# Performance work log

Measured on AMD Instinct MI355X. Metric: run time of the kernel, lower is better.

The kernel has to match this reference:

```python
import jax, jax.numpy as jnp
import numpy as np

B, S, D = 4, 2048, 1024
E, H, K = 32, 128, 2


def setup_inputs() -> dict:
    key = jax.random.key(0)
    k1, k2, k3, k4 = jax.random.split(key, 4)
    scale_d = 1.0 / np.sqrt(D)
    scale_h = 1.0 / np.sqrt(H)
    return {
        "x": jax.random.normal(k1, (B, S, D), dtype=jnp.float32),
        "w_sel": jax.random.normal(k2, (E, D), dtype=jnp.float32) * scale_d,      # router Linear weight [E, D]
        "w_keys": jax.random.normal(k3, (E, D, H), dtype=jnp.float32) * scale_d,  # per-expert up-proj
        "w_values": jax.random.normal(k4, (E, H, D), dtype=jnp.float32) * scale_h, # per-expert down-proj
        "k": K,
    }


def reference(x, w_sel, w_keys, w_values, k):
    # Router: sigmoid gating + top-k expert selection per token.
    sel = jax.nn.sigmoid(jnp.einsum('bsd,ed->bse', x, w_sel))      # [B,S,E]
    sel_val, sel_idx = jax.lax.top_k(sel, k)                       # [B,S,k]
    n_exp = w_sel.shape[0]
    # Dense gate matrix: gate[b,s,e] = sum of sel_val over heads routed to e
    # (top_k indices are distinct, so this matches the per-head accumulation).
    gate = jnp.sum(jax.nn.one_hot(sel_idx, n_exp, dtype=x.dtype) * sel_val[..., None], axis=-2)  # [B,S,E]
    # Expert up-projection + ReLU for all experts (dense equivalent of the
    # per-token gathered keys[expert_idx](token); unselected experts are
    # zeroed by the gate so the math is identical).
    scores = jax.nn.relu(jnp.einsum('bsd,edh->bseh', x, w_keys))   # [B,S,E,H]
    weighted = scores * gate[..., None]                            # [B,S,E,H]
    out = jnp.einsum('bseh,ehd->bsd', weighted, w_values)          # [B,S,D]
    return out
```

## Files before the change

kernel.cpp:

```cpp
#include <hip/hip_runtime.h>
#include <cstdint>
#include <cstddef>

#define NTOK 8192
#define DIM  1024
#define NEXP 32
#define NH   128
#define TT   32
#define NSLOT 32
#define BK   128
#define RT   32
#define LCAP 1024
#define NRB  (NTOK / RT)

typedef __attribute__((ext_vector_type(8))) short short8;
typedef __attribute__((ext_vector_type(4))) float float4_;

static __device__ __forceinline__ unsigned short f2bf(float f) {
  unsigned u = __float_as_uint(f);
  return (unsigned short)((u + 0x7fffu + ((u >> 16) & 1u)) >> 16);
}
static __device__ __forceinline__ float bf2f(unsigned short h) {
  return __uint_as_float(((unsigned)h) << 16);
}
static __device__ __forceinline__ void gload_lds16(const unsigned short* g,
                                                   unsigned short* l) {
  __builtin_amdgcn_global_load_lds(
      (const __attribute__((address_space(1))) unsigned int*)(const void*)g,
      (__attribute__((address_space(3))) unsigned int*)(void*)l, 16, 0, 0);
}

__global__ __launch_bounds__(256) void prep_router_kernel(
    const float* __restrict__ x, const float* __restrict__ w_sel,
    const float* __restrict__ w_keys, const float* __restrict__ w_values,
    unsigned short* __restrict__ xbf, unsigned short* __restrict__ wk_t,
    unsigned short* __restrict__ wv_t,
    int* __restrict__ counts, unsigned* __restrict__ list)
{
  __shared__ __align__(16) char smem[22656];
  const int bid = blockIdx.x;
  const int tid = threadIdx.x;

  if (bid >= NRB) {
    float (*tile)[65] = (float (*)[65])smem;
    const int lb = bid - NRB;
    const float* src; unsigned short* dst; int R, C, e, t, tpc;
    if (lb < 1024) { src = w_keys;   dst = wk_t; R = DIM; C = NH;  e = lb >> 5;          t = lb & 31; tpc = 2; }
    else           { src = w_values; dst = wv_t; R = NH;  C = DIM; e = (lb - 1024) >> 5; t = (lb - 1024) & 31; tpc = 16; }
    const int r0 = (t / tpc) * 64;
    const int c0 = (t % tpc) * 64;
    const float* s = src + (size_t)e * R * C;
    unsigned short* d = dst + (size_t)e * R * C;

    const int i  = tid >> 2;
    const int j0 = (tid & 3) * 16;
    #pragma unroll
    for (int k4 = 0; k4 < 4; ++k4) {
      float4 v = *(const float4*)(s + (size_t)(r0 + i) * C + c0 + j0 + k4 * 4);
      tile[i][j0 + k4 * 4 + 0] = v.x;
      tile[i][j0 + k4 * 4 + 1] = v.y;
      tile[i][j0 + k4 * 4 + 2] = v.z;
      tile[i][j0 + k4 * 4 + 3] = v.w;
    }
    __syncthreads();
    unsigned pk[8];
    #pragma unroll
    for (int k = 0; k < 8; ++k) {
      unsigned lo = f2bf(tile[j0 + 2 * k][i]);
      unsigned hi = f2bf(tile[j0 + 2 * k + 1][i]);
      pk[k] = lo | (hi << 16);
    }
    uint4 u0; u0.x = pk[0]; u0.y = pk[1]; u0.z = pk[2]; u0.w = pk[3];
    uint4 u1; u1.x = pk[4]; u1.y = pk[5]; u1.z = pk[6]; u1.w = pk[7];
    unsigned short* dp = d + (size_t)(c0 + i) * R + r0 + j0;
    *(uint4*)(dp)     = u0;
    *(uint4*)(dp + 8) = u1;
    return;
  }

  float (*xs_t)[36] = (float (*)[36])smem;
  float (*ws_t)[36] = (float (*)[36])(smem + 9216);
  float (*S)[33]    = (float (*)[33])(smem + 18432);
  float (*red)[64][16] = (float (*)[64][16])smem;

  const int tok0 = bid * RT;
  const int wv   = tid >> 6;
  const int lane = tid & 63;
  const int tr   = tid >> 3;
  const int i8   = tid & 7;
  const int d8   = i8 * 8;
  const int swzW = i8 << 2;
  const int tg4  = (lane & 7) * 4;
  const int eg4  = (lane >> 3) * 4;
  const int dlo  = wv * 16;

  float acc[16];
  #pragma unroll
  for (int k = 0; k < 16; ++k) acc[k] = 0.f;

  float4 a0, a1, b0, b1;
  {
    const float* xp = x + (size_t)(tok0 + tr) * DIM + d8;
    a0 = *(const float4*)(xp);
    a1 = *(const float4*)(xp + 4);
    const float* wp = w_sel + (size_t)tr * DIM + d8;
    b0 = *(const float4*)(wp);
    b1 = *(const float4*)(wp + 4);
  }

  for (int c = 0; c < 16; ++c) {
    const int dc = c * 64;

    {
      const int colx = tr ^ swzW;
      xs_t[d8 + 0][colx] = a0.x; xs_t[d8 + 1][colx] = a0.y;
      xs_t[d8 + 2][colx] = a0.z; xs_t[d8 + 3][colx] = a0.w;
      xs_t[d8 + 4][colx] = a1.x; xs_t[d8 + 5][colx] = a1.y;
      xs_t[d8 + 6][colx] = a1.z; xs_t[d8 + 7][colx] = a1.w;
      ws_t[d8 + 0][colx] = b0.x; ws_t[d8 + 1][colx] = b0.y;
      ws_t[d8 + 2][colx] = b0.z; ws_t[d8 + 3][colx] = b0.w;
      ws_t[d8 + 4][colx] = b1.x; ws_t[d8 + 5][colx] = b1.y;
      ws_t[d8 + 6][colx] = b1.z; ws_t[d8 + 7][colx] = b1.w;
      uint4 u;
      u.x = (unsigned)f2bf(a0.x) | ((unsigned)f2bf(a0.y) << 16);
      u.y = (unsigned)f2bf(a0.z) | ((unsigned)f2bf(a0.w) << 16);
      u.z = (unsigned)f2bf(a1.x) | ((unsigned)f2bf(a1.y) << 16);
      u.w = (unsigned)f2bf(a1.z) | ((unsigned)f2bf(a1.w) << 16);
      *(uint4*)(xbf + (size_t)(tok0 + tr) * DIM + dc + d8) = u;
    }
    __syncthreads();

    if (c < 15) {
      const float* xp = x + (size_t)(tok0 + tr) * DIM + dc + 64 + d8;
      a0 = *(const float4*)(xp);
      a1 = *(const float4*)(xp + 4);
      const float* wp = w_sel + (size_t)tr * DIM + dc + 64 + d8;
      b0 = *(const float4*)(wp);
      b1 = *(const float4*)(wp + 4);
    }

    #pragma unroll
    for (int dd = 0; dd < 16; ++dd) {
      const int d  = dlo + dd;
      const int sz = (d >> 3) << 2;
      float4 xv = *(const float4*)&xs_t[d][tg4 ^ sz];
      float4 w4 = *(const float4*)&ws_t[d][eg4 ^ sz];
      acc[0]  = fmaf(w4.x, xv.x, acc[0]);  acc[1]  = fmaf(w4.x, xv.y, acc[1]);
      acc[2]  = fmaf(w4.x, xv.z, acc[2]);  acc[3]  = fmaf(w4.x, xv.w, acc[3]);
      acc[4]  = fmaf(w4.y, xv.x, acc[4]);  acc[5]  = fmaf(w4.y, xv.y, acc[5]);
      acc[6]  = fmaf(w4.y, xv.z, acc[6]);  acc[7]  = fmaf(w4.y, xv.w, acc[7]);
      acc[8]  = fmaf(w4.z, xv.x, acc[8]);  acc[9]  = fmaf(w4.z, xv.y, acc[9]);
      acc[10] = fmaf(w4.z, xv.z, acc[10]); acc[11] = fmaf(w4.z, xv.w, acc[11]);
      acc[12] = fmaf(w4.w, xv.x, acc[12]); acc[13] = fmaf(w4.w, xv.y, acc[13]);
      acc[14] = fmaf(w4.w, xv.z, acc[14]); acc[15] = fmaf(w4.w, xv.w, acc[15]);
    }
    __syncthreads();
  }

  #pragma unroll
  for (int ei = 0; ei < 4; ++ei) {
    float4 v; v.x = acc[ei * 4 + 0]; v.y = acc[ei * 4 + 1];
    v.z = acc[ei * 4 + 2]; v.w = acc[ei * 4 + 3];
    *(float4*)&red[wv][lane][ei * 4] = v;
  }
  __syncthreads();

  {
    const int eg2 = tid >> 5, tg2 = (tid >> 2) & 7, ei2 = tid & 3;
    const int cls = eg2 * 8 + tg2;
    float4 s4; s4.x = 0.f; s4.y = 0.f; s4.z = 0.f; s4.w = 0.f;
    #pragma unroll
    for (int w = 0; w < 4; ++w) {
      float4 v = *(const float4*)&red[w][cls][ei2 * 4];
      s4.x += v.x; s4.y += v.y; s4.z += v.z; s4.w += v.w;
    }
    S[tg2 * 4 + 0][eg2 * 4 + ei2] = s4.x;
    S[tg2 * 4 + 1][eg2 * 4 + ei2] = s4.y;
    S[tg2 * 4 + 2][eg2 * 4 + ei2] = s4.z;
    S[tg2 * 4 + 3][eg2 * 4 + ei2] = s4.w;
  }
  __syncthreads();

  if (tid < RT) {
    const int t = tid;
    float m1 = -1e30f, m2 = -1e30f;
    int i1 = 0, i2 = 0;
    for (int ee = 0; ee < NEXP; ++ee) {
      float v = S[t][ee];
      if (v > m1)      { m2 = m1; i2 = i1; m1 = v; i1 = ee; }
      else if (v > m2) { m2 = v; i2 = ee; }
    }
    const int token = tok0 + t;
    float g1 = 1.f / (1.f + __expf(-m1));
    float g2 = 1.f / (1.f + __expf(-m2));
    unsigned e1 = ((unsigned)f2bf(g1) << 16) | ((unsigned)token << 1);
    unsigned e2 = ((unsigned)f2bf(g2) << 16) | ((unsigned)token << 1) | 1u;
    int p1 = atomicAdd(&counts[i1], 1);
    if (p1 < LCAP) list[i1 * LCAP + p1] = e1;
    int p2 = atomicAdd(&counts[i2], 1);
    if (p2 < LCAP) list[i2 * LCAP + p2] = e2;
  }
}

__global__ __launch_bounds__(256, 4) void ffn_kernel(
    const unsigned short* __restrict__ xbf,
    const unsigned short* __restrict__ wk_t,
    const unsigned short* __restrict__ wv_t,
    float* __restrict__ out,
    unsigned short* __restrict__ cont,
    const int* __restrict__ counts, const unsigned* __restrict__ list,
    int use_cont)
{
  const int bid = blockIdx.x;
  const int e   = bid & 31;
  const int cnt = min(counts[e], LCAP);
  const int t0  = (bid >> 5) * TT;
  if (t0 >= cnt) return;

  __shared__ __align__(16) unsigned short uni[8448];
  __shared__ unsigned short ss[TT][NH + 8];
  __shared__ int   toks[TT];
  __shared__ float gates[TT];
  unsigned short (*xsf)[4096] = (unsigned short (*)[4096])uni;
  unsigned short (*st)[264]   = (unsigned short (*)[264])uni;

  const int tid  = threadIdx.x;
  const int wave = tid >> 6;
  const int lane = tid & 63;
  const int quad = lane >> 4;
  const int l16  = lane & 15;

  const unsigned short* wkb = wk_t + (size_t)e * NH * DIM;
  const unsigned short* wvb = wv_t + (size_t)e * DIM * NH;
  const int n_tok = min(TT, cnt - t0);

  if (tid < TT) {
    int valid = tid < n_tok;
    unsigned en = valid ? list[e * LCAP + t0 + tid] : 0u;
    toks[tid]  = valid ? (int)(en & 0xffffu) : -1;
    gates[tid] = valid ? bf2f((unsigned short)(en >> 16)) : 0.f;
  }
  __syncthreads();

  const int smt  = wave >> 1;
  const int skk0 = (wave & 1) * 2;
  {
    int sl   = toks[smt * 16 + l16];
    int gtok = (sl < 0) ? 0 : (sl >> 1);
    const unsigned short* gsrc = xbf + (size_t)gtok * DIM + quad * 8;

    #pragma unroll
    for (int i2 = 0; i2 < 2; ++i2)
      gload_lds16(gsrc + (skk0 + i2) * 32, &xsf[0][(smt * 4 + skk0 + i2) * 512]);
    __syncthreads();

    float4_ acc[2][2];
    #pragma unroll
    for (int mt = 0; mt < 2; ++mt)
      #pragma unroll
      for (int nt = 0; nt < 2; ++nt) acc[mt][nt] = (float4_){0.f, 0.f, 0.f, 0.f};

    for (int ci = 0; ci < 8; ++ci) {
      const int dc = ci * BK;
      if (ci < 7) {
        const int nb = (ci + 1) & 1;
        #pragma unroll
        for (int i2 = 0; i2 < 2; ++i2)
          gload_lds16(gsrc + dc + BK + (skk0 + i2) * 32,
                      &xsf[nb][(smt * 4 + skk0 + i2) * 512]);
      }
      short8 b[4][2];
      #pragma unroll
      for (int kk = 0; kk < 4; ++kk)
        #pragma unroll
        for (int nt = 0; nt < 2; ++nt)
          b[kk][nt] = *(const short8*)(wkb +
              (size_t)(wave * 32 + nt * 16 + l16) * DIM + dc + kk * 32 + quad * 8);

      const unsigned short* xb = &xsf[ci & 1][0];
      #pragma unroll
      for (int kk = 0; kk < 4; ++kk) {
        #pragma unroll
        for (int mt = 0; mt < 2; ++mt) {
          short8 a = *(const short8*)(xb + (mt * 4 + kk) * 512 + lane * 8);
          #pragma unroll
          for (int nt = 0; nt < 2; ++nt)
            acc[mt][nt] = __builtin_amdgcn_mfma_f32_16x16x32_bf16(a, b[kk][nt], acc[mt][nt], 0, 0, 0);
        }
      }
      __syncthreads();
    }

    #pragma unroll
    for (int mt = 0; mt < 2; ++mt)
      #pragma unroll
      for (int nt = 0; nt < 2; ++nt)
        #pragma unroll
        for (int r = 0; r < 4; ++r) {
          int row = mt * 16 + quad * 4 + r;
          float v = fmaxf(acc[mt][nt][r], 0.f) * gates[row];
          ss[row][wave * 32 + nt * 16 + l16] = f2bf(v);
        }
  }
  __syncthreads();

  #pragma unroll 1
  for (int nc = 0; nc < 4; ++nc) {
    const int colbase = wave * 256 + nc * 64;
    float4_ o[2][4];
    #pragma unroll
    for (int mt = 0; mt < 2; ++mt)
      #pragma unroll
      for (int nt = 0; nt < 4; ++nt) o[mt][nt] = (float4_){0.f, 0.f, 0.f, 0.f};

    #pragma unroll
    for (int kk = 0; kk < 4; ++kk) {
      short8 bk[4];
      #pragma unroll
      for (int nt = 0; nt < 4; ++nt)
        bk[nt] = *(const short8*)(wvb +
            (size_t)(colbase + nt * 16 + l16) * NH + kk * 32 + quad * 8);
      short8 a0 = *(const short8*)&ss[l16][kk * 32 + quad * 8];
      short8 a1 = *(const short8*)&ss[16 + l16][kk * 32 + quad * 8];
      #pragma unroll
      for (int nt = 0; nt < 4; ++nt) {
        o[0][nt] = __builtin_amdgcn_mfma_f32_16x16x32_bf16(a0, bk[nt], o[0][nt], 0, 0, 0);
        o[1][nt] = __builtin_amdgcn_mfma_f32_16x16x32_bf16(a1, bk[nt], o[1][nt], 0, 0, 0);
      }
    }

    if (use_cont) {
      #pragma unroll
      for (int mt = 0; mt < 2; ++mt)
        #pragma unroll
        for (int nt = 0; nt < 4; ++nt)
          #pragma unroll
          for (int r = 0; r < 4; ++r)
            st[mt * 16 + quad * 4 + r][wave * 64 + nt * 16 + l16] = f2bf(o[mt][nt][r]);
      __syncthreads();
      #pragma unroll
      for (int q = 0; q < 4; ++q) {
        int idx = q * 256 + tid;
        int row = idx >> 5, seg = idx & 31;
        if (row < n_tok) {
          int sl2 = toks[row];
          size_t base = ((size_t)((sl2 & 1) * NTOK + (sl2 >> 1))) * DIM
                        + (seg >> 3) * 256 + nc * 64 + (seg & 7) * 8;
          *(short8*)&cont[base] = *(const short8*)&st[row][seg * 8];
        }
      }
      __syncthreads();
    } else {
      #pragma unroll
      for (int mt = 0; mt < 2; ++mt)
        #pragma unroll
        for (int r = 0; r < 4; ++r) {
          int row = mt * 16 + quad * 4 + r;
          if (row < n_tok) {
            size_t base = (size_t)(toks[row] >> 1) * DIM + colbase;
            #pragma unroll
            for (int nt = 0; nt < 4; ++nt)
              unsafeAtomicAdd(&out[base + nt * 16 + l16], o[mt][nt][r]);
          }
        }
    }
  }
}

__global__ __launch_bounds__(256) void combine_kernel(
    const unsigned short* __restrict__ cont, float* __restrict__ out)
{
  size_t i = ((size_t)blockIdx.x * 256 + threadIdx.x) * 8;
  uint4 a = *(const uint4*)(cont + i);
  uint4 b = *(const uint4*)(cont + (size_t)NTOK * DIM + i);
  float4 r0, r1;
  r0.x = bf2f((unsigned short)(a.x & 0xffff)) + bf2f((unsigned short)(b.x & 0xffff));
  r0.y = bf2f((unsigned short)(a.x >> 16))    + bf2f((unsigned short)(b.x >> 16));
  r0.z = bf2f((unsigned short)(a.y & 0xffff)) + bf2f((unsigned short)(b.y & 0xffff));
  r0.w = bf2f((unsigned short)(a.y >> 16))    + bf2f((unsigned short)(b.y >> 16));
  r1.x = bf2f((unsigned short)(a.z & 0xffff)) + bf2f((unsigned short)(b.z & 0xffff));
  r1.y = bf2f((unsigned short)(a.z >> 16))    + bf2f((unsigned short)(b.z >> 16));
  r1.z = bf2f((unsigned short)(a.w & 0xffff)) + bf2f((unsigned short)(b.w & 0xffff));
  r1.w = bf2f((unsigned short)(a.w >> 16))    + bf2f((unsigned short)(b.w >> 16));
  *(float4*)(out + i) = r0;
  *(float4*)(out + i + 4) = r1;
}

extern "C" void kernel_launch(void* const* d_in, const int* in_sizes, int n_in,
                              void* d_out, int out_size, void* d_ws, size_t ws_size,
                              hipStream_t stream) {
  (void)in_sizes; (void)n_in;
  const float* x        = (const float*)d_in[0];
  const float* w_sel    = (const float*)d_in[1];
  const float* w_keys   = (const float*)d_in[2];
  const float* w_values = (const float*)d_in[3];
  float* out = (float*)d_out;

  char* ws = (char*)d_ws;
  size_t off = 0;
  int*            counts = (int*)(ws + off);            off += 4096;
  unsigned*       list   = (unsigned*)(ws + off);       off += (size_t)NEXP * LCAP * 4;
  unsigned short* wk_t   = (unsigned short*)(ws + off); off += (size_t)NEXP * NH * DIM * 2;
  unsigned short* wv_t   = (unsigned short*)(ws + off); off += (size_t)NEXP * NH * DIM * 2;
  unsigned short* xbf    = (unsigned short*)(ws + off); off += (size_t)NTOK * DIM * 2;
  unsigned short* cont   = (unsigned short*)(ws + off);
  size_t need_full = off + (size_t)2 * NTOK * DIM * 2;
  const int use_cont = (ws_size >= need_full) ? 1 : 0;

  hipMemsetAsync(counts, 0, NEXP * sizeof(int), stream);

  prep_router_kernel<<<NRB + 2048, 256, 0, stream>>>(x, w_sel, w_keys, w_values,
                                                     xbf, wk_t, wv_t, counts, list);

  if (!use_cont)
    hipMemsetAsync(out, 0, (size_t)out_size * sizeof(float), stream);

  ffn_kernel<<<NEXP * NSLOT, 256, 0, stream>>>(xbf, wk_t, wv_t, out, cont,
                                               counts, list, use_cont);

  if (use_cont)
    combine_kernel<<<NTOK * DIM / (256 * 8), 256, 0, stream>>>(cont, out);
}
```

Before: 212.2 us.

## Halve FFN token tile to 16 and move x bf16 conversion to separate blocks

```diff
diff --git a/kernel.cpp b/kernel.cpp
--- a/kernel.cpp
+++ b/kernel.cpp
@@ -6,12 +6,14 @@
 #define DIM  1024
 #define NEXP 32
 #define NH   128
-#define TT   32
-#define NSLOT 32
+#define TT   16
+#define NSLOT 64
 #define BK   128
 #define RT   32
 #define LCAP 1024
 #define NRB  (NTOK / RT)
+#define NTRB 2048
+#define NCVB 512
 
 typedef __attribute__((ext_vector_type(8))) short short8;
 typedef __attribute__((ext_vector_type(4))) float float4_;
@@ -41,6 +43,30 @@
   const int bid = blockIdx.x;
   const int tid = threadIdx.x;
 
+  if (bid >= NRB + NTRB) {
+    const int lb = bid - NRB - NTRB;
+    #pragma unroll
+    for (int q = 0; q < 4; ++q) {
+      const size_t off = (size_t)lb * 16384 + (size_t)q * 4096 + (size_t)tid * 16;
+      float4 v0 = *(const float4*)(x + off);
+      float4 v1 = *(const float4*)(x + off + 4);
+      float4 v2 = *(const float4*)(x + off + 8);
+      float4 v3 = *(const float4*)(x + off + 12);
+      uint4 u0, u1;
+      u0.x = (unsigned)f2bf(v0.x) | ((unsigned)f2bf(v0.y) << 16);
+      u0.y = (unsigned)f2bf(v0.z) | ((unsigned)f2bf(v0.w) << 16);
+      u0.z = (unsigned)f2bf(v1.x) | ((unsigned)f2bf(v1.y) << 16);
+      u0.w = (unsigned)f2bf(v1.z) | ((unsigned)f2bf(v1.w) << 16);
+      u1.x = (unsigned)f2bf(v2.x) | ((unsigned)f2bf(v2.y) << 16);
+      u1.y = (unsigned)f2bf(v2.z) | ((unsigned)f2bf(v2.w) << 16);
+      u1.z = (unsigned)f2bf(v3.x) | ((unsigned)f2bf(v3.y) << 16);
+      u1.w = (unsigned)f2bf(v3.z) | ((unsigned)f2bf(v3.w) << 16);
+      *(uint4*)(xbf + off)     = u0;
+      *(uint4*)(xbf + off + 8) = u1;
+    }
+    return;
+  }
+
   if (bid >= NRB) {
     float (*tile)[65] = (float (*)[65])smem;
     const int lb = bid - NRB;
@@ -121,12 +147,6 @@
       ws_t[d8 + 2][colx] = b0.z; ws_t[d8 + 3][colx] = b0.w;
       ws_t[d8 + 4][colx] = b1.x; ws_t[d8 + 5][colx] = b1.y;
       ws_t[d8 + 6][colx] = b1.z; ws_t[d8 + 7][colx] = b1.w;
-      uint4 u;
-      u.x = (unsigned)f2bf(a0.x) | ((unsigned)f2bf(a0.y) << 16);
-      u.y = (unsigned)f2bf(a0.z) | ((unsigned)f2bf(a0.w) << 16);
-      u.z = (unsigned)f2bf(a1.x) | ((unsigned)f2bf(a1.y) << 16);
-      u.w = (unsigned)f2bf(a1.z) | ((unsigned)f2bf(a1.w) << 16);
-      *(uint4*)(xbf + (size_t)(tok0 + tr) * DIM + dc + d8) = u;
     }
     __syncthreads();
 
@@ -217,11 +237,11 @@
   const int t0  = (bid >> 5) * TT;
   if (t0 >= cnt) return;
 
-  __shared__ __align__(16) unsigned short uni[8448];
+  __shared__ __align__(16) unsigned short uni[4224];
   __shared__ unsigned short ss[TT][NH + 8];
   __shared__ int   toks[TT];
   __shared__ float gates[TT];
-  unsigned short (*xsf)[4096] = (unsigned short (*)[4096])uni;
+  unsigned short (*xsf)[2048] = (unsigned short (*)[2048])uni;
   unsigned short (*st)[264]   = (unsigned short (*)[264])uni;
 
   const int tid  = threadIdx.x;
@@ -242,33 +262,23 @@
   }
   __syncthreads();
 
-  const int smt  = wave >> 1;
-  const int skk0 = (wave & 1) * 2;
   {
-    int sl   = toks[smt * 16 + l16];
+    int sl   = toks[l16];
     int gtok = (sl < 0) ? 0 : (sl >> 1);
     const unsigned short* gsrc = xbf + (size_t)gtok * DIM + quad * 8;
 
-    #pragma unroll
-    for (int i2 = 0; i2 < 2; ++i2)
-      gload_lds16(gsrc + (skk0 + i2) * 32, &xsf[0][(smt * 4 + skk0 + i2) * 512]);
+    gload_lds16(gsrc + wave * 32, &xsf[0][wave * 512]);
     __syncthreads();
 
-    float4_ acc[2][2];
-    #pragma unroll
-    for (int mt = 0; mt < 2; ++mt)
-      #pragma unroll
-      for (int nt = 0; nt < 2; ++nt) acc[mt][nt] = (float4_){0.f, 0.f, 0.f, 0.f};
+    float4_ acc[2];
+    acc[0] = (float4_){0.f, 0.f, 0.f, 0.f};
+    acc[1] = (float4_){0.f, 0.f, 0.f, 0.f};
 
     for (int ci = 0; ci < 8; ++ci) {
       const int dc = ci * BK;
-      if (ci < 7) {
-        const int nb = (ci + 1) & 1;
-        #pragma unroll
-        for (int i2 = 0; i2 < 2; ++i2)
-          gload_lds16(gsrc + dc + BK + (skk0 + i2) * 32,
-                      &xsf[nb][(smt * 4 + skk0 + i2) * 512]);
-      }
+      if (ci < 7)
+        gload_lds16(gsrc + dc + BK + wave * 32, &xsf[(ci + 1) & 1][wave * 512]);
+
       short8 b[4][2];
       #pragma unroll
       for (int kk = 0; kk < 4; ++kk)
@@ -280,38 +290,30 @@
       const unsigned short* xb = &xsf[ci & 1][0];
       #pragma unroll
       for (int kk = 0; kk < 4; ++kk) {
-        #pragma unroll
-        for (int mt = 0; mt < 2; ++mt) {
-          short8 a = *(const short8*)(xb + (mt * 4 + kk) * 512 + lane * 8);
-          #pragma unroll
-          for (int nt = 0; nt < 2; ++nt)
-            acc[mt][nt] = __builtin_amdgcn_mfma_f32_16x16x32_bf16(a, b[kk][nt], acc[mt][nt], 0, 0, 0);
-        }
+        short8 a = *(const short8*)(xb + kk * 512 + lane * 8);
+        acc[0] = __builtin_amdgcn_mfma_f32_16x16x32_bf16(a, b[kk][0], acc[0], 0, 0, 0);
+        acc[1] = __builtin_amdgcn_mfma_f32_16x16x32_bf16(a, b[kk][1], acc[1], 0, 0, 0);
       }
       __syncthreads();
     }
 
     #pragma unroll
-    for (int mt = 0; mt < 2; ++mt)
-      #pragma unroll
-      for (int nt = 0; nt < 2; ++nt)
-        #pragma unroll
-        for (int r = 0; r < 4; ++r) {
-          int row = mt * 16 + quad * 4 + r;
-          float v = fmaxf(acc[mt][nt][r], 0.f) * gates[row];
-          ss[row][wave * 32 + nt * 16 + l16] = f2bf(v);
-        }
+    for (int nt = 0; nt < 2; ++nt)
+      #pragma unroll
+      for (int r = 0; r < 4; ++r) {
+        int row = quad * 4 + r;
+        float v = fmaxf(acc[nt][r], 0.f) * gates[row];
+        ss[row][wave * 32 + nt * 16 + l16] = f2bf(v);
+      }
   }
   __syncthreads();
 
   #pragma unroll 1
   for (int nc = 0; nc < 4; ++nc) {
     const int colbase = wave * 256 + nc * 64;
-    float4_ o[2][4];
-    #pragma unroll
-    for (int mt = 0; mt < 2; ++mt)
-      #pragma unroll
-      for (int nt = 0; nt < 4; ++nt) o[mt][nt] = (float4_){0.f, 0.f, 0.f, 0.f};
+    float4_ o[4];
+    #pragma unroll
+    for (int nt = 0; nt < 4; ++nt) o[nt] = (float4_){0.f, 0.f, 0.f, 0.f};
 
     #pragma unroll
     for (int kk = 0; kk < 4; ++kk) {
@@ -321,25 +323,20 @@
         bk[nt] = *(const short8*)(wvb +
             (size_t)(colbase + nt * 16 + l16) * NH + kk * 32 + quad * 8);
       short8 a0 = *(const short8*)&ss[l16][kk * 32 + quad * 8];
-      short8 a1 = *(const short8*)&ss[16 + l16][kk * 32 + quad * 8];
-      #pragma unroll
-      for (int nt = 0; nt < 4; ++nt) {
-        o[0][nt] = __builtin_amdgcn_mfma_f32_16x16x32_bf16(a0, bk[nt], o[0][nt], 0, 0, 0);
-        o[1][nt] = __builtin_amdgcn_mfma_f32_16x16x32_bf16(a1, bk[nt], o[1][nt], 0, 0, 0);
-      }
+      #pragma unroll
+      for (int nt = 0; nt < 4; ++nt)
+        o[nt] = __builtin_amdgcn_mfma_f32_16x16x32_bf16(a0, bk[nt], o[nt], 0, 0, 0);
     }
 
     if (use_cont) {
       #pragma unroll
-      for (int mt = 0; mt < 2; ++mt)
+      for (int nt = 0; nt < 4; ++nt)
         #pragma unroll
-        for (int nt = 0; nt < 4; ++nt)
-          #pragma unroll
-          for (int r = 0; r < 4; ++r)
-            st[mt * 16 + quad * 4 + r][wave * 64 + nt * 16 + l16] = f2bf(o[mt][nt][r]);
+        for (int r = 0; r < 4; ++r)
+          st[quad * 4 + r][wave * 64 + nt * 16 + l16] = f2bf(o[nt][r]);
       __syncthreads();
       #pragma unroll
-      for (int q = 0; q < 4; ++q) {
+      for (int q = 0; q < 2; ++q) {
         int idx = q * 256 + tid;
         int row = idx >> 5, seg = idx & 31;
         if (row < n_tok) {
@@ -352,17 +349,15 @@
       __syncthreads();
     } else {
       #pragma unroll
-      for (int mt = 0; mt < 2; ++mt)
-        #pragma unroll
-        for (int r = 0; r < 4; ++r) {
-          int row = mt * 16 + quad * 4 + r;
-          if (row < n_tok) {
-            size_t base = (size_t)(toks[row] >> 1) * DIM + colbase;
-            #pragma unroll
-            for (int nt = 0; nt < 4; ++nt)
-              unsafeAtomicAdd(&out[base + nt * 16 + l16], o[mt][nt][r]);
-          }
+      for (int r = 0; r < 4; ++r) {
+        int row = quad * 4 + r;
+        if (row < n_tok) {
+          size_t base = (size_t)(toks[row] >> 1) * DIM + colbase;
+          #pragma unroll
+          for (int nt = 0; nt < 4; ++nt)
+            unsafeAtomicAdd(&out[base + nt * 16 + l16], o[nt][r]);
         }
+      }
     }
   }
 }
@@ -409,8 +404,8 @@
 
   hipMemsetAsync(counts, 0, NEXP * sizeof(int), stream);
 
-  prep_router_kernel<<<NRB + 2048, 256, 0, stream>>>(x, w_sel, w_keys, w_values,
-                                                     xbf, wk_t, wv_t, counts, list);
+  prep_router_kernel<<<NRB + NTRB + NCVB, 256, 0, stream>>>(
+      x, w_sel, w_keys, w_values, xbf, wk_t, wv_t, counts, list);
 
   if (!use_cont)
     hipMemsetAsync(out, 0, (size_t)out_size * sizeof(float), stream);
```

New measurement: 242.7 us. +14.4%, slower.

## Split router GEMM over two D-halves and move top-2 selection to separate kernel

Applied to the files above, without the earlier changes.

```diff
diff --git a/kernel.cpp b/kernel.cpp
--- a/kernel.cpp
+++ b/kernel.cpp
@@ -11,7 +11,8 @@
 #define BK   128
 #define RT   32
 #define LCAP 1024
-#define NRB  (NTOK / RT)
+#define NRB  512
+#define NTRB 2048
 
 typedef __attribute__((ext_vector_type(8))) short short8;
 typedef __attribute__((ext_vector_type(4))) float float4_;
@@ -34,10 +35,9 @@
     const float* __restrict__ x, const float* __restrict__ w_sel,
     const float* __restrict__ w_keys, const float* __restrict__ w_values,
     unsigned short* __restrict__ xbf, unsigned short* __restrict__ wk_t,
-    unsigned short* __restrict__ wv_t,
-    int* __restrict__ counts, unsigned* __restrict__ list)
+    unsigned short* __restrict__ wv_t, float* __restrict__ logits_p)
 {
-  __shared__ __align__(16) char smem[22656];
+  __shared__ __align__(16) char smem[18432];
   const int bid = blockIdx.x;
   const int tid = threadIdx.x;
 
@@ -80,10 +80,13 @@
 
   float (*xs_t)[36] = (float (*)[36])smem;
   float (*ws_t)[36] = (float (*)[36])(smem + 9216);
-  float (*S)[33]    = (float (*)[33])(smem + 18432);
   float (*red)[64][16] = (float (*)[64][16])smem;
 
-  const int tok0 = bid * RT;
+  const int tg    = bid >> 1;
+  const int half  = bid & 1;
+  const int tok0  = tg * RT;
+  const int dbase = half * 512;
+
   const int wv   = tid >> 6;
   const int lane = tid & 63;
   const int tr   = tid >> 3;
@@ -100,16 +103,16 @@
 
   float4 a0, a1, b0, b1;
   {
-    const float* xp = x + (size_t)(tok0 + tr) * DIM + d8;
+    const float* xp = x + (size_t)(tok0 + tr) * DIM + dbase + d8;
     a0 = *(const float4*)(xp);
     a1 = *(const float4*)(xp + 4);
-    const float* wp = w_sel + (size_t)tr * DIM + d8;
+    const float* wp = w_sel + (size_t)tr * DIM + dbase + d8;
     b0 = *(const float4*)(wp);
     b1 = *(const float4*)(wp + 4);
   }
 
-  for (int c = 0; c < 16; ++c) {
-    const int dc = c * 64;
+  for (int c = 0; c < 8; ++c) {
+    const int dc = dbase + c * 64;
 
     {
       const int colx = tr ^ swzW;
@@ -130,7 +133,7 @@
     }
     __syncthreads();
 
-    if (c < 15) {
+    if (c < 7) {
       const float* xp = x + (size_t)(tok0 + tr) * DIM + dc + 64 + d8;
       a0 = *(const float4*)(xp);
       a1 = *(const float4*)(xp + 4);
@@ -174,32 +177,36 @@
       float4 v = *(const float4*)&red[w][cls][ei2 * 4];
       s4.x += v.x; s4.y += v.y; s4.z += v.z; s4.w += v.w;
     }
-    S[tg2 * 4 + 0][eg2 * 4 + ei2] = s4.x;
-    S[tg2 * 4 + 1][eg2 * 4 + ei2] = s4.y;
-    S[tg2 * 4 + 2][eg2 * 4 + ei2] = s4.z;
-    S[tg2 * 4 + 3][eg2 * 4 + ei2] = s4.w;
-  }
-  __syncthreads();
-
-  if (tid < RT) {
-    const int t = tid;
-    float m1 = -1e30f, m2 = -1e30f;
-    int i1 = 0, i2 = 0;
-    for (int ee = 0; ee < NEXP; ++ee) {
-      float v = S[t][ee];
-      if (v > m1)      { m2 = m1; i2 = i1; m1 = v; i1 = ee; }
-      else if (v > m2) { m2 = v; i2 = ee; }
-    }
-    const int token = tok0 + t;
-    float g1 = 1.f / (1.f + __expf(-m1));
-    float g2 = 1.f / (1.f + __expf(-m2));
-    unsigned e1 = ((unsigned)f2bf(g1) << 16) | ((unsigned)token << 1);
-    unsigned e2 = ((unsigned)f2bf(g2) << 16) | ((unsigned)token << 1) | 1u;
-    int p1 = atomicAdd(&counts[i1], 1);
-    if (p1 < LCAP) list[i1 * LCAP + p1] = e1;
-    int p2 = atomicAdd(&counts[i2], 1);
-    if (p2 < LCAP) list[i2 * LCAP + p2] = e2;
-  }
+    float* lp = logits_p + ((size_t)half * NEXP + eg2 * 4 + ei2) * NTOK
+              + tok0 + tg2 * 4;
+    float4 o; o.x = s4.x; o.y = s4.y; o.z = s4.z; o.w = s4.w;
+    *(float4*)lp = o;
+  }
+}
+
+__global__ __launch_bounds__(256) void top2_kernel(
+    const float* __restrict__ logits_p, int* __restrict__ counts,
+    unsigned* __restrict__ list)
+{
+  const int token = blockIdx.x * 256 + threadIdx.x;
+  const float* p = logits_p + token;
+
+  float m1 = -1e30f, m2 = -1e30f;
+  int i1 = 0, i2 = 0;
+  for (int e = 0; e < NEXP; ++e) {
+    float v = p[(size_t)(0 * NEXP + e) * NTOK]
+            + p[(size_t)(1 * NEXP + e) * NTOK];
+    if (v > m1)      { m2 = m1; i2 = i1; m1 = v; i1 = e; }
+    else if (v > m2) { m2 = v; i2 = e; }
+  }
+  float g1 = 1.f / (1.f + __expf(-m1));
+  float g2 = 1.f / (1.f + __expf(-m2));
+  unsigned e1 = ((unsigned)f2bf(g1) << 16) | ((unsigned)token << 1);
+  unsigned e2 = ((unsigned)f2bf(g2) << 16) | ((unsigned)token << 1) | 1u;
+  int p1 = atomicAdd(&counts[i1], 1);
+  if (p1 < LCAP) list[i1 * LCAP + p1] = e1;
+  int p2 = atomicAdd(&counts[i2], 1);
+  if (p2 < LCAP) list[i2 * LCAP + p2] = e2;
 }
 
 __global__ __launch_bounds__(256, 4) void ffn_kernel(
@@ -404,13 +411,16 @@
   unsigned short* wv_t   = (unsigned short*)(ws + off); off += (size_t)NEXP * NH * DIM * 2;
   unsigned short* xbf    = (unsigned short*)(ws + off); off += (size_t)NTOK * DIM * 2;
   unsigned short* cont   = (unsigned short*)(ws + off);
+  float* logits_p = (float*)cont;
   size_t need_full = off + (size_t)2 * NTOK * DIM * 2;
   const int use_cont = (ws_size >= need_full) ? 1 : 0;
 
   hipMemsetAsync(counts, 0, NEXP * sizeof(int), stream);
 
-  prep_router_kernel<<<NRB + 2048, 256, 0, stream>>>(x, w_sel, w_keys, w_values,
-                                                     xbf, wk_t, wv_t, counts, list);
+  prep_router_kernel<<<NRB + NTRB, 256, 0, stream>>>(
+      x, w_sel, w_keys, w_values, xbf, wk_t, wv_t, logits_p);
+
+  top2_kernel<<<NTOK / 256, 256, 0, stream>>>(logits_p, counts, list);
 
   if (!use_cont)
     hipMemsetAsync(out, 0, (size_t)out_size * sizeof(float), stream);
```

Result: slower. 216.4 us (+2.0%).
